# Performance work log

Hardware: AMD Instinct MI355X
Metric: run time of the kernel (lower is better)

Reference implementation:

```python
import jax, jax.numpy as jnp
import numpy as np

DEPTH = 2
EPS = 1e-12

def _l2norm(x, axis=-1):
    n = jnp.sqrt(jnp.sum(x * x, axis=axis, keepdims=True))
    return x / jnp.maximum(n, EPS)

def setup_inputs() -> dict:
    key = jax.random.key(0)
    k1, k2, k3, k4, k5 = jax.random.split(key, 5)
    N, D, R, E = 50000, 100, 1000, 800000
    features = jax.random.normal(k1, (N, D), dtype=jnp.float32)
    rel_emb = jax.random.normal(k2, (R, D), dtype=jnp.float32)
    none_relation = jax.random.normal(k3, (D,), dtype=jnp.float32)
    # edge list sorted by destination row (matches coalesced sparse layout
    # assumed by the original: softmax values align with edge order)
    rows = jnp.sort(jax.random.randint(k4, (E,), 0, N))
    cols = jax.random.randint(k5, (E,), 0, N)
    adj_index = jnp.stack([rows, cols], axis=1).astype(jnp.int64)
    return {"features": features, "rel_emb": rel_emb,
            "adj_index": adj_index, "none_relation": none_relation}

def reference(features, rel_emb, adj_index, none_relation):
    N = features.shape[0]
    rows = adj_index[:, 0]  # destination (softmax segment, scatter target)
    cols = adj_index[:, 1]  # neighbor (gather source)
    feats = jnp.tanh(features)
    outputs = [feats]
    nr = _l2norm(none_relation, axis=0)  # [D]
    for _ in range(DEPTH):
        neighs = feats[cols]                      # [E, D] gather
        score = -jnp.einsum('ed,d->e', _l2norm(neighs), nr)  # [E]
        # sparse softmax over each destination row's edges
        m = jax.ops.segment_max(score, rows, num_segments=N)
        e = jnp.exp(score - m[rows])
        denom = jax.ops.segment_sum(e, rows, num_segments=N)
        att = e / denom[rows]                     # [E]
        new_feats = jax.ops.segment_sum(neighs * att[:, None], rows,
                                        num_segments=N)  # [N, D]
        feats = jnp.tanh(new_feats)
        outputs.append(feats)
    return jnp.concatenate(outputs, axis=1)  # [N, D*(DEPTH+1)]
```

## Files before the change

kernel.cpp:

```cpp
#include <hip/hip_runtime.h>
#include <math.h>

#define D_FEAT 100
#define ROW_STRIDE 300
#define ROWQ 26
#define ROWB 208u

__device__ __forceinline__ float fast_tanh(float x) {
    float ax = fabsf(x);
    float e  = __expf(2.f * ax);
    float t  = 1.f - 2.f / (e + 1.f);
    return copysignf(t, x);
}

__device__ __forceinline__ unsigned pack_bf16x2(float a, float b) {
    unsigned ua = __float_as_uint(a);
    unsigned ub = __float_as_uint(b);
    ua += 0x7fffu + ((ua >> 16) & 1u);
    ub += 0x7fffu + ((ub >> 16) & 1u);
    return (ua >> 16) | (ub & 0xffff0000u);
}
__device__ __forceinline__ unsigned long long pack_bf16x4(float a, float b,
                                                          float c, float d) {
    return (unsigned long long)pack_bf16x2(a, b) |
           ((unsigned long long)pack_bf16x2(c, d) << 32);
}
__device__ __forceinline__ void unpack_bf16x4(unsigned long long u,
                                              float& x0, float& x1,
                                              float& x2, float& x3) {
    unsigned lo = (unsigned)u, hi = (unsigned)(u >> 32);
    x0 = __uint_as_float(lo << 16);
    x1 = __uint_as_float(lo & 0xffff0000u);
    x2 = __uint_as_float(hi << 16);
    x3 = __uint_as_float(hi & 0xffff0000u);
}
__device__ __forceinline__ void unpack2(unsigned u, float& lo, float& hi) {
    lo = __uint_as_float(u << 16);
    hi = __uint_as_float(u & 0xffff0000u);
}

__device__ __forceinline__ float half_reduce(float v) {
    #pragma unroll
    for (int off = 16; off; off >>= 1) v += __shfl_xor(v, off, 64);
    return v;
}

__global__ __launch_bounds__(256) void tanh_score_kernel(
    const float* __restrict__ features,
    float* __restrict__ out,
    unsigned long long* __restrict__ tab0,
    float* __restrict__ escore0,
    const float* __restrict__ none_rel,
    const int* __restrict__ adj,
    int* __restrict__ startArr,
    int E, int N)
{
    int gtid = blockIdx.x * blockDim.x + threadIdx.x;
    if (gtid <= N) {
        if (gtid == N) startArr[N] = E;
        else {
            int lo = 0, hi = E;
            while (lo < hi) {
                int mid = (lo + hi) >> 1;
                if (adj[2 * mid] < gtid) lo = mid + 1; else hi = mid;
            }
            startArr[gtid] = lo;
        }
    }

    int waveId = gtid >> 6;
    int lane = threadIdx.x & 63;
    int half = lane >> 5;
    int l    = lane & 31;
    int n    = waveId * 2 + half;
    const bool valid_n = (n < N);
    const bool fact = valid_n && (l >= 1) && (l <= 25);

    float x0 = 0.f, x1 = 0.f, x2 = 0.f, x3 = 0.f;
    if (fact) {
        float4 f = ((const float4*)(features + (size_t)n * D_FEAT))[l - 1];
        x0 = fast_tanh(f.x); x1 = fast_tanh(f.y);
        x2 = fast_tanh(f.z); x3 = fast_tanh(f.w);
        ((float4*)(out + (size_t)n * ROW_STRIDE))[l - 1] = make_float4(x0, x1, x2, x3);
        if (tab0) tab0[(size_t)n * ROWQ + l] = pack_bf16x4(x0, x1, x2, x3);
    }

    float nx = 0.f, ny = 0.f, nz = 0.f, nw = 0.f;
    if (l >= 1 && l <= 25) {
        float4 v = ((const float4*)none_rel)[l - 1];
        nx = v.x; ny = v.y; nz = v.z; nw = v.w;
    }
    float ss = half_reduce(nx * nx + ny * ny + nz * nz + nw * nw);
    float inv_nr = 1.f / fmaxf(sqrtf(ss), 1e-12f);

    float dot = half_reduce(x0 * nx + x1 * ny + x2 * nz + x3 * nw) * inv_nr;
    float sq  = half_reduce(x0 * x0 + x1 * x1 + x2 * x2 + x3 * x3);
    if (l == 0 && valid_n) {
        float es = __expf(-dot / fmaxf(sqrtf(sq), 1e-12f));
        if (tab0) tab0[(size_t)n * ROWQ] = (unsigned long long)__float_as_uint(es);
        else      escore0[n] = es;
    }
}

template <bool WRITE_TAB>
__global__ __launch_bounds__(256) void attn16_kernel(
    const unsigned long long* __restrict__ tab,
    float* __restrict__ outp,
    unsigned long long* __restrict__ tab_out,
    const int2* __restrict__ adj2,
    const int* __restrict__ start,
    const float* __restrict__ none_rel,
    int N)
{
    const int waveId = (int)((blockIdx.x * blockDim.x + threadIdx.x) >> 6);
    const int lane = threadIdx.x & 63;
    const int half = lane >> 5;
    const int l    = lane & 31;
    const int base = half << 5;
    const int n    = waveId * 2 + half;
    const bool valid_n = (n < N);

    const bool act  = (l < 26);
    const int  wh   = (act && l >= 13) ? 1 : 0;
    const int  sub  = act ? (l - 13 * wh) : 0;
    const bool actA = (l < 13);

    int e0 = 0, e1 = 0;
    if (valid_n) { e0 = start[n]; e1 = start[n + 1]; }
    const int deg = e1 - e0;
    int maxdeg = deg;
    { int o = __shfl_xor(maxdeg, 32, 64); maxdeg = maxdeg > o ? maxdeg : o; }

    int c0 = 0, c1 = 0;
    if (l < deg)      c0 = adj2[e0 + l].y;
    if (l + 32 < deg) c1 = adj2[e0 + l + 32].y;

    const char* tb = (const char*)tab;
    const size_t suboff = (size_t)(sub * 16);
    const int wsrc = base + 13 * wh;
    const int degw = deg - wh;

    float a0=0.f,a1=0.f,a2=0.f,a3=0.f,a4=0.f,a5=0.f,a6=0.f,a7=0.f;
    float d_acc = 0.f;

#define ATTN16_PASS(CSTAGE, I, SRC)                                           \
    {                                                                         \
        int c = __shfl((CSTAGE), base + (SRC) + wh, 64);                      \
        const uint4 v = *(const uint4*)(tb + (size_t)(unsigned)c * ROWB + suboff); \
        float w = __shfl(__uint_as_float(v.x), wsrc, 64);                     \
        w = ((I) < degw) ? w : 0.f;                                           \
        float p0,p1,p2,p3,p4,p5,p6,p7;                                        \
        unpack2(v.x,p0,p1); unpack2(v.y,p2,p3);                               \
        unpack2(v.z,p4,p5); unpack2(v.w,p6,p7);                               \
        if (sub == 0) { p0 = 0.f; p1 = 0.f; }           \
        a0 += w*p0; a1 += w*p1; a2 += w*p2; a3 += w*p3;                       \
        a4 += w*p4; a5 += w*p5; a6 += w*p6; a7 += w*p7;                       \
        d_acc += w;                                                           \
    }

    const int cap1 = maxdeg < 32 ? maxdeg : 32;
    for (int r = 0; r < cap1; r += 8) {
        #pragma unroll
        for (int j = 0; j < 4; ++j) {
            const int i = r + 2 * j;
            ATTN16_PASS(c0, i, i)
        }
    }
    const int cap2 = maxdeg < 64 ? maxdeg : 64;
    for (int r = 32; r < cap2; r += 8) {
        #pragma unroll
        for (int j = 0; j < 4; ++j) {
            const int i = r + 2 * j;
            ATTN16_PASS(c1, i, i - 32)
        }
    }
#undef ATTN16_PASS

    for (int e = e0 + 64; e < e1; ++e) {
        int c = adj2[e].y;
        const uint4 v = *(const uint4*)(tb + (size_t)(unsigned)c * ROWB + suboff);
        float w = __shfl(__uint_as_float(v.x), base, 64);
        float p0,p1,p2,p3,p4,p5,p6,p7;
        unpack2(v.x,p0,p1); unpack2(v.y,p2,p3);
        unpack2(v.z,p4,p5); unpack2(v.w,p6,p7);
        if (sub == 0) { p0 = 0.f; p1 = 0.f; }
        if (wh == 0) {
            a0 += w*p0; a1 += w*p1; a2 += w*p2; a3 += w*p3;
            a4 += w*p4; a5 += w*p5; a6 += w*p6; a7 += w*p7;
            d_acc += w;
        }
    }

    const int partner = base + (actA ? l + 13 : (act ? l - 13 : l));
    d_acc += __shfl(d_acc, partner, 64);
    a0 += __shfl(a0, partner, 64);
    a1 += __shfl(a1, partner, 64);
    a2 += __shfl(a2, partner, 64);
    a3 += __shfl(a3, partner, 64);
    a4 += __shfl(a4, partner, 64);
    a5 += __shfl(a5, partner, 64);
    a6 += __shfl(a6, partner, 64);
    a7 += __shfl(a7, partner, 64);

    const float inv_d = (deg > 0) ? 1.f / d_acc : 0.f;
    float r0 = fast_tanh(a0 * inv_d);
    float r1 = fast_tanh(a1 * inv_d);
    float r2 = fast_tanh(a2 * inv_d);
    float r3 = fast_tanh(a3 * inv_d);
    float r4 = fast_tanh(a4 * inv_d);
    float r5 = fast_tanh(a5 * inv_d);
    float r6 = fast_tanh(a6 * inv_d);
    float r7 = fast_tanh(a7 * inv_d);
    if (!actA) { r0=r1=r2=r3=r4=r5=r6=r7=0.f; }

    if (valid_n && actA) {
        float4* orow = (float4*)(outp + (size_t)n * ROW_STRIDE);
        if (l == 0) {
            orow[0] = make_float4(r4, r5, r6, r7);
        } else {
            orow[2*l - 1] = make_float4(r0, r1, r2, r3);
            orow[2*l]     = make_float4(r4, r5, r6, r7);
        }
        if constexpr (WRITE_TAB) {
            if (l > 0) {
                uint4* trow = (uint4*)((char*)tab_out + (size_t)n * ROWB);
                trow[l] = make_uint4(pack_bf16x2(r0,r1), pack_bf16x2(r2,r3),
                                     pack_bf16x2(r4,r5), pack_bf16x2(r6,r7));
            }
        }
    }

    if constexpr (WRITE_TAB) {
        float n0=0.f,n1=0.f,n2=0.f,n3=0.f,n4=0.f,n5=0.f,n6=0.f,n7=0.f;
        if (l == 0) {
            float4 v = ((const float4*)none_rel)[0];
            n4=v.x; n5=v.y; n6=v.z; n7=v.w;
        } else if (l < 13) {
            float4 u = *(const float4*)(none_rel + 8*l - 4);
            float4 v = *(const float4*)(none_rel + 8*l);
            n0=u.x; n1=u.y; n2=u.z; n3=u.w;
            n4=v.x; n5=v.y; n6=v.z; n7=v.w;
        }
        float ss = half_reduce(n0*n0+n1*n1+n2*n2+n3*n3+n4*n4+n5*n5+n6*n6+n7*n7);
        float inv_nr = 1.f / fmaxf(sqrtf(ss), 1e-12f);
        float dot = half_reduce(r0*n0+r1*n1+r2*n2+r3*n3+r4*n4+r5*n5+r6*n6+r7*n7) * inv_nr;
        float sq  = half_reduce(r0*r0+r1*r1+r2*r2+r3*r3+r4*r4+r5*r5+r6*r6+r7*r7);
        if (l == 0 && valid_n) {
            float es = __expf(-dot / fmaxf(sqrtf(sq), 1e-12f));
            uint4* trow = (uint4*)((char*)tab_out + (size_t)n * ROWB);
            trow[0] = make_uint4(__float_as_uint(es), 0u,
                                 pack_bf16x2(r4,r5), pack_bf16x2(r6,r7));
        }
    }
}

template <bool TAB>
__global__ __launch_bounds__(256) void attn_kernel(
    const void* __restrict__ prev,
    float* __restrict__ outp,
    unsigned long long* __restrict__ tab_out,
    const int2* __restrict__ adj2,
    const int* __restrict__ start,
    const float* __restrict__ escore_in,
    float* __restrict__ escore_out,
    const float* __restrict__ none_rel,
    int N)
{
    int waveId = (int)((blockIdx.x * blockDim.x + threadIdx.x) >> 6);
    int lane = threadIdx.x & 63;
    int half = lane >> 5;
    int l    = lane & 31;
    int n    = waveId * 2 + half;
    const bool valid_n = (n < N);
    const bool fact = valid_n && (l >= 1) && (l <= 25);
    const int base = half << 5;

    int e0 = 0, e1 = 0;
    if (valid_n) { e0 = start[n]; e1 = start[n + 1]; }
    const int deg = e1 - e0;

    int   c0 = 0, c1 = 0;
    float w0 = 0.f, w1 = 0.f;
    if (l < deg)      { c0 = adj2[e0 + l].y;      if (!TAB) w0 = escore_in[c0]; }
    if (l + 32 < deg) { c1 = adj2[e0 + l + 32].y; if (!TAB) w1 = escore_in[c1]; }

    int maxdeg = deg;
    { int o = __shfl_xor(maxdeg, 32, 64); maxdeg = maxdeg > o ? maxdeg : o; }

    const float* pf32 = (const float*)prev;

    float d_acc = 0.f, a0 = 0.f, a1 = 0.f, a2 = 0.f, a3 = 0.f;
    const int cap1 = maxdeg < 32 ? maxdeg : 32;
    for (int r = 0; r < cap1; r += 8) {
        #pragma unroll
        for (int j = 0; j < 8; ++j) {
            int   i = r + j;
            int   c = __shfl(c0, base + i, 64);
            float w = __shfl(w0, base + i, 64);
            float p0 = 0.f, p1 = 0.f, p2 = 0.f, p3 = 0.f;
            if (fact && (i < deg)) {
                float4 v = ((const float4*)(pf32 + (size_t)c * ROW_STRIDE))[l - 1];
                p0 = v.x; p1 = v.y; p2 = v.z; p3 = v.w;
            }
            if (i >= deg) w = 0.f;
            d_acc += w;
            a0 += w * p0; a1 += w * p1; a2 += w * p2; a3 += w * p3;
        }
    }
    const int cap2 = maxdeg < 64 ? maxdeg : 64;
    for (int r = 32; r < cap2; r += 8) {
        #pragma unroll
        for (int j = 0; j < 8; ++j) {
            int   i = r + j;
            int   c = __shfl(c1, base + i - 32, 64);
            float w = __shfl(w1, base + i - 32, 64);
            float p0 = 0.f, p1 = 0.f, p2 = 0.f, p3 = 0.f;
            if (fact && (i < deg)) {
                float4 v = ((const float4*)(pf32 + (size_t)c * ROW_STRIDE))[l - 1];
                p0 = v.x; p1 = v.y; p2 = v.z; p3 = v.w;
            }
            if (i >= deg) w = 0.f;
            d_acc += w;
            a0 += w * p0; a1 += w * p1; a2 += w * p2; a3 += w * p3;
        }
    }
    for (int e = e0 + 64; e < e1; ++e) {
        int c = adj2[e].y;
        float w = escore_in[c];
        float p0 = 0.f, p1 = 0.f, p2 = 0.f, p3 = 0.f;
        if (fact) {
            float4 v = ((const float4*)(pf32 + (size_t)c * ROW_STRIDE))[l - 1];
            p0 = v.x; p1 = v.y; p2 = v.z; p3 = v.w;
        }
        d_acc += w;
        a0 += w * p0; a1 += w * p1; a2 += w * p2; a3 += w * p3;
    }

    const float inv_d = (deg > 0) ? 1.f / d_acc : 0.f;
    float r0 = fast_tanh(a0 * inv_d);
    float r1 = fast_tanh(a1 * inv_d);
    float r2 = fast_tanh(a2 * inv_d);
    float r3 = fast_tanh(a3 * inv_d);
    if (fact) {
        ((float4*)(outp + (size_t)n * ROW_STRIDE))[l - 1] = make_float4(r0, r1, r2, r3);
    } else {
        r0 = r1 = r2 = r3 = 0.f;
    }

    if (escore_out) {
        float nx = 0.f, ny = 0.f, nz = 0.f, nw = 0.f;
        if (l >= 1 && l <= 25) {
            float4 v = ((const float4*)none_rel)[l - 1];
            nx = v.x; ny = v.y; nz = v.z; nw = v.w;
        }
        float ss = half_reduce(nx * nx + ny * ny + nz * nz + nw * nw);
        float inv_nr = 1.f / fmaxf(sqrtf(ss), 1e-12f);
        float dot = half_reduce(r0 * nx + r1 * ny + r2 * nz + r3 * nw) * inv_nr;
        float sq  = half_reduce(r0 * r0 + r1 * r1 + r2 * r2 + r3 * r3);
        if (l == 0 && valid_n) {
            float es = __expf(-dot / fmaxf(sqrtf(sq), 1e-12f));
            escore_out[n] = es;
        }
    }
}

extern "C" void kernel_launch(void* const* d_in, const int* in_sizes, int n_in,
                              void* d_out, int out_size, void* d_ws, size_t ws_size,
                              hipStream_t stream) {
    const float* features = (const float*)d_in[0];
    const int*   adj      = (const int*)d_in[2];
    const float* none_rel = (const float*)d_in[3];
    float* out = (float*)d_out;

    const int N = in_sizes[0] / D_FEAT;
    const int E = in_sizes[2] / 2;

    size_t off = 0;
    auto take = [&](size_t bytes) { size_t o = off; off = (off + bytes + 15) & ~(size_t)15; return o; };
    char* w = (char*)d_ws;
    int*   start   = (int*)  (w + take(sizeof(int)   * (size_t)(N + 1)));
    float* escore0 = (float*)(w + take(sizeof(float) * (size_t)N));
    float* escore1 = (float*)(w + take(sizeof(float) * (size_t)N));
    size_t tab_off0 = take(sizeof(unsigned long long) * (size_t)N * ROWQ);
    size_t tab_off1 = take(sizeof(unsigned long long) * (size_t)N * ROWQ);
    const bool use_tab = (ws_size >= off);
    unsigned long long* tab0 = use_tab ? (unsigned long long*)(w + tab_off0) : nullptr;
    unsigned long long* tab1 = use_tab ? (unsigned long long*)(w + tab_off1) : nullptr;

    const int pairs = (N + 1) / 2;
    const int node_blocks = (pairs * 64 + 255) / 256;
    const int2* adj2 = (const int2*)adj;

    tanh_score_kernel<<<node_blocks, 256, 0, stream>>>(features, out, tab0,
                                                       escore0, none_rel,
                                                       adj, start, E, N);
    if (use_tab) {
        attn16_kernel<true><<<node_blocks, 256, 0, stream>>>(
            tab0, out + D_FEAT, tab1, adj2, start, none_rel, N);
        attn16_kernel<false><<<node_blocks, 256, 0, stream>>>(
            tab1, out + 2 * D_FEAT, nullptr, adj2, start, none_rel, N);
    } else {
        attn_kernel<false><<<node_blocks, 256, 0, stream>>>(
            out, out + D_FEAT, nullptr, adj2, start, escore0, escore1, none_rel, N);
        attn_kernel<false><<<node_blocks, 256, 0, stream>>>(
            out + D_FEAT, out + 2 * D_FEAT, nullptr, adj2, start, escore1, nullptr, none_rel, N);
    }
}
```

Baseline: 157.3 us.

## Switch gather table to fp16 and move attention scores to a separate array

The packed neighbor table changes from bf16 with the exp-score embedded in slot 0 to a plain fp16 row of 100 features padded to 208 bytes. Scores are now read from a separate per-node float array, gathered once per edge into registers, and the denominator is computed with one half-wave reduction. Per-edge work drops the score shuffle, the masking and the unpack bit-ops, in exchange for an extra scattered 4-byte load per edge. fp16 also changes the rounding behaviour compared with bf16.

```diff
diff --git a/kernel.cpp b/kernel.cpp
--- a/kernel.cpp
+++ b/kernel.cpp
@@ -1,9 +1,9 @@
 #include <hip/hip_runtime.h>
+#include <hip/hip_fp16.h>
 #include <math.h>
 
 #define D_FEAT 100
 #define ROW_STRIDE 300
-#define ROWQ 26
 #define ROWB 208u
 
 __device__ __forceinline__ float fast_tanh(float x) {
@@ -13,30 +13,10 @@
     return copysignf(t, x);
 }
 
-__device__ __forceinline__ unsigned pack_bf16x2(float a, float b) {
-    unsigned ua = __float_as_uint(a);
-    unsigned ub = __float_as_uint(b);
-    ua += 0x7fffu + ((ua >> 16) & 1u);
-    ub += 0x7fffu + ((ub >> 16) & 1u);
-    return (ua >> 16) | (ub & 0xffff0000u);
-}
-__device__ __forceinline__ unsigned long long pack_bf16x4(float a, float b,
-                                                          float c, float d) {
-    return (unsigned long long)pack_bf16x2(a, b) |
-           ((unsigned long long)pack_bf16x2(c, d) << 32);
-}
-__device__ __forceinline__ void unpack_bf16x4(unsigned long long u,
-                                              float& x0, float& x1,
-                                              float& x2, float& x3) {
-    unsigned lo = (unsigned)u, hi = (unsigned)(u >> 32);
-    x0 = __uint_as_float(lo << 16);
-    x1 = __uint_as_float(lo & 0xffff0000u);
-    x2 = __uint_as_float(hi << 16);
-    x3 = __uint_as_float(hi & 0xffff0000u);
-}
-__device__ __forceinline__ void unpack2(unsigned u, float& lo, float& hi) {
-    lo = __uint_as_float(u << 16);
-    hi = __uint_as_float(u & 0xffff0000u);
+__device__ __forceinline__ unsigned pack_f16x2(float a, float b) {
+    __half2 h = __floats2half2_rn(a, b);
+    union { __half2 h; unsigned u; } cvt; cvt.h = h;
+    return cvt.u;
 }
 
 __device__ __forceinline__ float half_reduce(float v) {
@@ -70,9 +50,9 @@
 
     int waveId = gtid >> 6;
     int lane = threadIdx.x & 63;
-    int half = lane >> 5;
+    int h32  = lane >> 5;
     int l    = lane & 31;
-    int n    = waveId * 2 + half;
+    int n    = waveId * 2 + h32;
     const bool valid_n = (n < N);
     const bool fact = valid_n && (l >= 1) && (l <= 25);
 
@@ -82,7 +62,16 @@
         x0 = fast_tanh(f.x); x1 = fast_tanh(f.y);
         x2 = fast_tanh(f.z); x3 = fast_tanh(f.w);
         ((float4*)(out + (size_t)n * ROW_STRIDE))[l - 1] = make_float4(x0, x1, x2, x3);
-        if (tab0) tab0[(size_t)n * ROWQ + l] = pack_bf16x4(x0, x1, x2, x3);
+    }
+    if (tab0 && valid_n) {
+        char* row = (char*)tab0 + (size_t)n * ROWB;
+        if (l >= 1 && l <= 25) {
+            unsigned long long q = (unsigned long long)pack_f16x2(x0, x1) |
+                                   ((unsigned long long)pack_f16x2(x2, x3) << 32);
+            *(unsigned long long*)(row + 8 * (l - 1)) = q;
+        } else if (l == 26) {
+            *(unsigned long long*)(row + 200) = 0ULL;
+        }
     }
 
     float nx = 0.f, ny = 0.f, nz = 0.f, nw = 0.f;
@@ -97,8 +86,7 @@
     float sq  = half_reduce(x0 * x0 + x1 * x1 + x2 * x2 + x3 * x3);
     if (l == 0 && valid_n) {
         float es = __expf(-dot / fmaxf(sqrtf(sq), 1e-12f));
-        if (tab0) tab0[(size_t)n * ROWQ] = (unsigned long long)__float_as_uint(es);
-        else      escore0[n] = es;
+        escore0[n] = es;
     }
 }
 
@@ -109,15 +97,17 @@
     unsigned long long* __restrict__ tab_out,
     const int2* __restrict__ adj2,
     const int* __restrict__ start,
+    const float* __restrict__ esc_in,
+    float* __restrict__ esc_out,
     const float* __restrict__ none_rel,
     int N)
 {
     const int waveId = (int)((blockIdx.x * blockDim.x + threadIdx.x) >> 6);
     const int lane = threadIdx.x & 63;
-    const int half = lane >> 5;
+    const int h32  = lane >> 5;
     const int l    = lane & 31;
-    const int base = half << 5;
-    const int n    = waveId * 2 + half;
+    const int base = h32 << 5;
+    const int n    = waveId * 2 + h32;
     const bool valid_n = (n < N);
 
     const bool act  = (l < 26);
@@ -131,68 +121,69 @@
     int maxdeg = deg;
     { int o = __shfl_xor(maxdeg, 32, 64); maxdeg = maxdeg > o ? maxdeg : o; }
 
-    int c0 = 0, c1 = 0;
-    if (l < deg)      c0 = adj2[e0 + l].y;
-    if (l + 32 < deg) c1 = adj2[e0 + l + 32].y;
+    int   c0 = 0, c1 = 0;
+    float w0 = 0.f, w1 = 0.f;
+    if (l < deg)      { c0 = adj2[e0 + l].y;      w0 = esc_in[c0]; }
+    if (l + 32 < deg) { c1 = adj2[e0 + l + 32].y; w1 = esc_in[c1]; }
+
+    float dsum = half_reduce(w0 + w1);
 
     const char* tb = (const char*)tab;
-    const size_t suboff = (size_t)(sub * 16);
-    const int wsrc = base + 13 * wh;
-    const int degw = deg - wh;
+    const unsigned suboff = (unsigned)(sub * 16);
 
     float a0=0.f,a1=0.f,a2=0.f,a3=0.f,a4=0.f,a5=0.f,a6=0.f,a7=0.f;
-    float d_acc = 0.f;
-
-#define ATTN16_PASS(CSTAGE, I, SRC)                                           \
+
+#define ATTN16_PASS(CSTAGE, WSTAGE, SRC)                                      \
     {                                                                         \
-        int c = __shfl((CSTAGE), base + (SRC) + wh, 64);                      \
-        const uint4 v = *(const uint4*)(tb + (size_t)(unsigned)c * ROWB + suboff); \
-        float w = __shfl(__uint_as_float(v.x), wsrc, 64);                     \
-        w = ((I) < degw) ? w : 0.f;                                           \
-        float p0,p1,p2,p3,p4,p5,p6,p7;                                        \
-        unpack2(v.x,p0,p1); unpack2(v.y,p2,p3);                               \
-        unpack2(v.z,p4,p5); unpack2(v.w,p6,p7);                               \
-        if (sub == 0) { p0 = 0.f; p1 = 0.f; }           \
-        a0 += w*p0; a1 += w*p1; a2 += w*p2; a3 += w*p3;                       \
-        a4 += w*p4; a5 += w*p5; a6 += w*p6; a7 += w*p7;                       \
-        d_acc += w;                                                           \
+        int   c = __shfl((CSTAGE), base + (SRC) + wh, 64);                    \
+        float w = __shfl((WSTAGE), base + (SRC) + wh, 64);                    \
+        const uint4 v = *(const uint4*)(tb + (size_t)((unsigned)c * ROWB + suboff)); \
+        const __half2* hv = (const __half2*)&v;                               \
+        a0 = fmaf(__low2float(hv[0]),  w, a0);                                \
+        a1 = fmaf(__high2float(hv[0]), w, a1);                                \
+        a2 = fmaf(__low2float(hv[1]),  w, a2);                                \
+        a3 = fmaf(__high2float(hv[1]), w, a3);                                \
+        a4 = fmaf(__low2float(hv[2]),  w, a4);                                \
+        a5 = fmaf(__high2float(hv[2]), w, a5);                                \
+        a6 = fmaf(__low2float(hv[3]),  w, a6);                                \
+        a7 = fmaf(__high2float(hv[3]), w, a7);                                \
     }
 
     const int cap1 = maxdeg < 32 ? maxdeg : 32;
     for (int r = 0; r < cap1; r += 8) {
         #pragma unroll
         for (int j = 0; j < 4; ++j) {
-            const int i = r + 2 * j;
-            ATTN16_PASS(c0, i, i)
+            ATTN16_PASS(c0, w0, r + 2 * j)
         }
     }
     const int cap2 = maxdeg < 64 ? maxdeg : 64;
     for (int r = 32; r < cap2; r += 8) {
         #pragma unroll
         for (int j = 0; j < 4; ++j) {
-            const int i = r + 2 * j;
-            ATTN16_PASS(c1, i, i - 32)
+            ATTN16_PASS(c1, w1, r + 2 * j - 32)
         }
     }
 #undef ATTN16_PASS
 
     for (int e = e0 + 64; e < e1; ++e) {
-        int c = adj2[e].y;
-        const uint4 v = *(const uint4*)(tb + (size_t)(unsigned)c * ROWB + suboff);
-        float w = __shfl(__uint_as_float(v.x), base, 64);
-        float p0,p1,p2,p3,p4,p5,p6,p7;
-        unpack2(v.x,p0,p1); unpack2(v.y,p2,p3);
-        unpack2(v.z,p4,p5); unpack2(v.w,p6,p7);
-        if (sub == 0) { p0 = 0.f; p1 = 0.f; }
-        if (wh == 0) {
-            a0 += w*p0; a1 += w*p1; a2 += w*p2; a3 += w*p3;
-            a4 += w*p4; a5 += w*p5; a6 += w*p6; a7 += w*p7;
-            d_acc += w;
-        }
+        int   c = adj2[e].y;
+        float w = esc_in[c];
+        const uint4 v = *(const uint4*)(tb + (size_t)((unsigned)c * ROWB + suboff));
+        const __half2* hv = (const __half2*)&v;
+        if (actA) {
+            a0 = fmaf(__low2float(hv[0]),  w, a0);
+            a1 = fmaf(__high2float(hv[0]), w, a1);
+            a2 = fmaf(__low2float(hv[1]),  w, a2);
+            a3 = fmaf(__high2float(hv[1]), w, a3);
+            a4 = fmaf(__low2float(hv[2]),  w, a4);
+            a5 = fmaf(__high2float(hv[2]), w, a5);
+            a6 = fmaf(__low2float(hv[3]),  w, a6);
+            a7 = fmaf(__high2float(hv[3]), w, a7);
+        }
+        dsum += w;
     }
 
     const int partner = base + (actA ? l + 13 : (act ? l - 13 : l));
-    d_acc += __shfl(d_acc, partner, 64);
     a0 += __shfl(a0, partner, 64);
     a1 += __shfl(a1, partner, 64);
     a2 += __shfl(a2, partner, 64);
@@ -202,7 +193,7 @@
     a6 += __shfl(a6, partner, 64);
     a7 += __shfl(a7, partner, 64);
 
-    const float inv_d = (deg > 0) ? 1.f / d_acc : 0.f;
+    const float inv_d = (deg > 0) ? 1.f / dsum : 0.f;
     float r0 = fast_tanh(a0 * inv_d);
     float r1 = fast_tanh(a1 * inv_d);
     float r2 = fast_tanh(a2 * inv_d);
@@ -215,31 +206,25 @@
 
     if (valid_n && actA) {
         float4* orow = (float4*)(outp + (size_t)n * ROW_STRIDE);
-        if (l == 0) {
-            orow[0] = make_float4(r4, r5, r6, r7);
-        } else {
-            orow[2*l - 1] = make_float4(r0, r1, r2, r3);
-            orow[2*l]     = make_float4(r4, r5, r6, r7);
-        }
+        orow[2*l] = make_float4(r0, r1, r2, r3);
+        if (l < 12)
+            orow[2*l + 1] = make_float4(r4, r5, r6, r7);
         if constexpr (WRITE_TAB) {
-            if (l > 0) {
-                uint4* trow = (uint4*)((char*)tab_out + (size_t)n * ROWB);
-                trow[l] = make_uint4(pack_bf16x2(r0,r1), pack_bf16x2(r2,r3),
-                                     pack_bf16x2(r4,r5), pack_bf16x2(r6,r7));
-            }
+            uint4* trow = (uint4*)((char*)tab_out + (size_t)n * ROWB);
+            trow[l] = make_uint4(pack_f16x2(r0, r1), pack_f16x2(r2, r3),
+                                 pack_f16x2(r4, r5), pack_f16x2(r6, r7));
         }
     }
 
     if constexpr (WRITE_TAB) {
         float n0=0.f,n1=0.f,n2=0.f,n3=0.f,n4=0.f,n5=0.f,n6=0.f,n7=0.f;
-        if (l == 0) {
-            float4 v = ((const float4*)none_rel)[0];
-            n4=v.x; n5=v.y; n6=v.z; n7=v.w;
-        } else if (l < 13) {
-            float4 u = *(const float4*)(none_rel + 8*l - 4);
-            float4 v = *(const float4*)(none_rel + 8*l);
+        if (actA) {
+            float4 u = *(const float4*)(none_rel + 8 * l);
             n0=u.x; n1=u.y; n2=u.z; n3=u.w;
-            n4=v.x; n5=v.y; n6=v.z; n7=v.w;
+            if (l < 12) {
+                float4 v2 = *(const float4*)(none_rel + 8 * l + 4);
+                n4=v2.x; n5=v2.y; n6=v2.z; n7=v2.w;
+            }
         }
         float ss = half_reduce(n0*n0+n1*n1+n2*n2+n3*n3+n4*n4+n5*n5+n6*n6+n7*n7);
         float inv_nr = 1.f / fmaxf(sqrtf(ss), 1e-12f);
@@ -247,18 +232,14 @@
         float sq  = half_reduce(r0*r0+r1*r1+r2*r2+r3*r3+r4*r4+r5*r5+r6*r6+r7*r7);
         if (l == 0 && valid_n) {
             float es = __expf(-dot / fmaxf(sqrtf(sq), 1e-12f));
-            uint4* trow = (uint4*)((char*)tab_out + (size_t)n * ROWB);
-            trow[0] = make_uint4(__float_as_uint(es), 0u,
-                                 pack_bf16x2(r4,r5), pack_bf16x2(r6,r7));
-        }
-    }
-}
-
-template <bool TAB>
-__global__ __launch_bounds__(256) void attn_kernel(
-    const void* __restrict__ prev,
+            esc_out[n] = es;
+        }
+    }
+}
+
+__global__ __launch_bounds__(256) void attn_f32_kernel(
+    const float* __restrict__ prev,
     float* __restrict__ outp,
-    unsigned long long* __restrict__ tab_out,
     const int2* __restrict__ adj2,
     const int* __restrict__ start,
     const float* __restrict__ escore_in,
@@ -268,12 +249,12 @@
 {
     int waveId = (int)((blockIdx.x * blockDim.x + threadIdx.x) >> 6);
     int lane = threadIdx.x & 63;
-    int half = lane >> 5;
+    int h32  = lane >> 5;
     int l    = lane & 31;
-    int n    = waveId * 2 + half;
+    int n    = waveId * 2 + h32;
     const bool valid_n = (n < N);
     const bool fact = valid_n && (l >= 1) && (l <= 25);
-    const int base = half << 5;
+    const int base = h32 << 5;
 
     int e0 = 0, e1 = 0;
     if (valid_n) { e0 = start[n]; e1 = start[n + 1]; }
@@ -281,13 +262,11 @@
 
     int   c0 = 0, c1 = 0;
     float w0 = 0.f, w1 = 0.f;
-    if (l < deg)      { c0 = adj2[e0 + l].y;      if (!TAB) w0 = escore_in[c0]; }
-    if (l + 32 < deg) { c1 = adj2[e0 + l + 32].y; if (!TAB) w1 = escore_in[c1]; }
+    if (l < deg)      { c0 = adj2[e0 + l].y;      w0 = escore_in[c0]; }
+    if (l + 32 < deg) { c1 = adj2[e0 + l + 32].y; w1 = escore_in[c1]; }
 
     int maxdeg = deg;
     { int o = __shfl_xor(maxdeg, 32, 64); maxdeg = maxdeg > o ? maxdeg : o; }
-
-    const float* pf32 = (const float*)prev;
 
     float d_acc = 0.f, a0 = 0.f, a1 = 0.f, a2 = 0.f, a3 = 0.f;
     const int cap1 = maxdeg < 32 ? maxdeg : 32;
@@ -299,7 +278,7 @@
             float w = __shfl(w0, base + i, 64);
             float p0 = 0.f, p1 = 0.f, p2 = 0.f, p3 = 0.f;
             if (fact && (i < deg)) {
-                float4 v = ((const float4*)(pf32 + (size_t)c * ROW_STRIDE))[l - 1];
+                float4 v = ((const float4*)(prev + (size_t)c * ROW_STRIDE))[l - 1];
                 p0 = v.x; p1 = v.y; p2 = v.z; p3 = v.w;
             }
             if (i >= deg) w = 0.f;
@@ -316,7 +295,7 @@
             float w = __shfl(w1, base + i - 32, 64);
             float p0 = 0.f, p1 = 0.f, p2 = 0.f, p3 = 0.f;
             if (fact && (i < deg)) {
-                float4 v = ((const float4*)(pf32 + (size_t)c * ROW_STRIDE))[l - 1];
+                float4 v = ((const float4*)(prev + (size_t)c * ROW_STRIDE))[l - 1];
                 p0 = v.x; p1 = v.y; p2 = v.z; p3 = v.w;
             }
             if (i >= deg) w = 0.f;
@@ -329,7 +308,7 @@
         float w = escore_in[c];
         float p0 = 0.f, p1 = 0.f, p2 = 0.f, p3 = 0.f;
         if (fact) {
-            float4 v = ((const float4*)(pf32 + (size_t)c * ROW_STRIDE))[l - 1];
+            float4 v = ((const float4*)(prev + (size_t)c * ROW_STRIDE))[l - 1];
             p0 = v.x; p1 = v.y; p2 = v.z; p3 = v.w;
         }
         d_acc += w;
@@ -381,8 +360,8 @@
     int*   start   = (int*)  (w + take(sizeof(int)   * (size_t)(N + 1)));
     float* escore0 = (float*)(w + take(sizeof(float) * (size_t)N));
     float* escore1 = (float*)(w + take(sizeof(float) * (size_t)N));
-    size_t tab_off0 = take(sizeof(unsigned long long) * (size_t)N * ROWQ);
-    size_t tab_off1 = take(sizeof(unsigned long long) * (size_t)N * ROWQ);
+    size_t tab_off0 = take((size_t)N * ROWB);
+    size_t tab_off1 = take((size_t)N * ROWB);
     const bool use_tab = (ws_size >= off);
     unsigned long long* tab0 = use_tab ? (unsigned long long*)(w + tab_off0) : nullptr;
     unsigned long long* tab1 = use_tab ? (unsigned long long*)(w + tab_off1) : nullptr;
@@ -396,13 +375,13 @@
                                                        adj, start, E, N);
     if (use_tab) {
         attn16_kernel<true><<<node_blocks, 256, 0, stream>>>(
-            tab0, out + D_FEAT, tab1, adj2, start, none_rel, N);
+            tab0, out + D_FEAT, tab1, adj2, start, escore0, escore1, none_rel, N);
         attn16_kernel<false><<<node_blocks, 256, 0, stream>>>(
-            tab1, out + 2 * D_FEAT, nullptr, adj2, start, none_rel, N);
+            tab1, out + 2 * D_FEAT, nullptr, adj2, start, escore1, nullptr, none_rel, N);
     } else {
-        attn_kernel<false><<<node_blocks, 256, 0, stream>>>(
-            out, out + D_FEAT, nullptr, adj2, start, escore0, escore1, none_rel, N);
-        attn_kernel<false><<<node_blocks, 256, 0, stream>>>(
-            out + D_FEAT, out + 2 * D_FEAT, nullptr, adj2, start, escore1, nullptr, none_rel, N);
-    }
-}
+        attn_f32_kernel<<<node_blocks, 256, 0, stream>>>(
+            out, out + D_FEAT, adj2, start, escore0, escore1, none_rel, N);
+        attn_f32_kernel<<<node_blocks, 256, 0, stream>>>(
+            out + D_FEAT, out + 2 * D_FEAT, adj2, start, escore1, nullptr, none_rel, N);
+    }
+}
```

Measured after the change: 159.4 us. About the same (+1.3%).
